# Performance work log

Hardware: AMD Instinct MI355X
Metric: run time of the kernel (lower is better)

Reference implementation:

```python
import jax, jax.numpy as jnp
import numpy as np

T, N, D, H = 128, 512, 1024, 1024
LN_EPS = 1e-5


def setup_inputs() -> dict:
    key = jax.random.key(0)
    ks = jax.random.split(key, 6)
    x = jax.random.normal(ks[0], (T * N, D), jnp.float32)
    hxs = jax.random.normal(ks[1], (N, 1, H), jnp.float32)
    # binary done-masks (float, mostly 1.0 = keep hidden state, 0.0 = episode reset)
    masks = (jax.random.uniform(ks[2], (T * N, 1)) < 0.95).astype(jnp.float32)
    s = 1.0 / np.sqrt(H)
    # PyTorch GRU packed gates, order (r, z, n): weight_ih_l0 [3H, D], weight_hh_l0 [3H, H]
    W_ih = jax.random.normal(ks[3], (3 * H, D), jnp.float32) * s
    W_hh = jax.random.normal(ks[4], (3 * H, H), jnp.float32) * s
    b_ih = jnp.zeros((3 * H,), jnp.float32)  # module inits biases to 0
    b_hh = jnp.zeros((3 * H,), jnp.float32)
    gamma = jnp.ones((H,), jnp.float32)
    beta = jnp.zeros((H,), jnp.float32)
    return dict(x=x, hxs=hxs, masks=masks, W_ih=W_ih, W_hh=W_hh,
                b_ih=b_ih, b_hh=b_hh, gamma=gamma, beta=beta)


def reference(x, hxs, masks, W_ih, W_hh, b_ih, b_hh, gamma, beta):
    TN = x.shape[0]
    Nn = hxs.shape[0]
    Tt = TN // Nn
    Hd = hxs.shape[-1]
    xs = x.reshape(Tt, Nn, -1)          # [T, N, D]
    m = masks.reshape(Tt, Nn)           # [T, N]
    # Chunk starts per source: t=0 plus every t>=1 where (masks[t] == 1).any().
    # At a chunk start the hidden state is multiplied by masks[t] (broadcast over layers);
    # a scan with a per-step conditional mask-multiply is exactly equivalent to the
    # torch loop over chunks.
    reset = jnp.concatenate([jnp.ones((1,), bool), jnp.any(m[1:] == 1.0, axis=-1)])
    # Batch the input projection across all T*N tokens (one big GEMM): [T, N, 3H]
    xp = jnp.einsum('tnd,gd->tng', xs, W_ih) + b_ih
    h0 = hxs[:, 0, :]                   # recurrent_N == 1 -> [N, H]

    def step(h, inp):
        xp_t, m_t, r_t = inp
        h = jnp.where(r_t, h * m_t[:, None], h)
        hp = h @ W_hh.T + b_hh          # [N, 3H]
        xr, xz, xn = jnp.split(xp_t, 3, axis=-1)
        hr, hz, hn = jnp.split(hp, 3, axis=-1)
        r = jax.nn.sigmoid(xr + hr)
        z = jax.nn.sigmoid(xz + hz)
        n = jnp.tanh(xn + r * hn)
        h_new = (1.0 - z) * n + z * h
        return h_new, h_new

    h_last, outs = jax.lax.scan(step, h0, (xp, m, reset))
    y = outs.reshape(Tt * Nn, Hd)
    # LayerNorm over last dim
    mu = y.mean(-1, keepdims=True)
    var = y.var(-1, keepdims=True)
    y = (y - mu) * jax.lax.rsqrt(var + LN_EPS) * gamma + beta
    return y, h_last[:, None, :]
```

## Files before the change

kernel.cpp:

```cpp
#include <hip/hip_runtime.h>

#define T_STEPS 128
#define N_B     512
#define D_IN    1024
#define H_DIM   1024
#define G_DIM   3072
#define M_ALL   (T_STEPS * N_B)
#define BAR_STRIDE 64

typedef short          s8v  __attribute__((ext_vector_type(8)));
typedef float          f4v  __attribute__((ext_vector_type(4)));
typedef unsigned short u4v  __attribute__((ext_vector_type(4)));

__device__ __forceinline__ unsigned short f2bf(float f) {
  union { float f; unsigned u; } v; v.f = f;
  unsigned r = v.u + 0x7FFFu + ((v.u >> 16) & 1u);
  return (unsigned short)(r >> 16);
}
__device__ __forceinline__ float bf2f(unsigned short h) {
  union { unsigned u; float f; } v; v.u = ((unsigned)h) << 16;
  return v.f;
}
__device__ __forceinline__ void async16(const void* g, void* l) {
  __builtin_amdgcn_global_load_lds(
      (const __attribute__((address_space(1))) unsigned*)g,
      (__attribute__((address_space(3))) unsigned*)l, 16, 0, 0);
}
__device__ __forceinline__ void async16_sc0(const void* g, void* l) {
  __builtin_amdgcn_global_load_lds(
      (const __attribute__((address_space(1))) unsigned*)g,
      (__attribute__((address_space(3))) unsigned*)l, 16, 0, 1);
}
__device__ __forceinline__ float sigmoidf_(float x) { return 1.f / (1.f + __expf(-x)); }
__device__ __forceinline__ float tanhf_(float x)    { return 1.f - 2.f / (1.f + __expf(2.f * x)); }

__global__ void cvt_bf16(const float* __restrict__ in, unsigned short* __restrict__ out, long n4) {
  long i = (long)blockIdx.x * blockDim.x + threadIdx.x;
  long stride = (long)gridDim.x * blockDim.x;
  for (; i < n4; i += stride) {
    f4v v = *(const f4v*)(in + i * 4);
    u4v o;
    #pragma unroll
    for (int e = 0; e < 4; ++e) o[e] = f2bf(v[e]);
    *(u4v*)(out + i * 4) = o;
  }
}

__global__ void reset_kernel(const float* __restrict__ masks, int* __restrict__ reset) {
  const int t = blockIdx.x;
  __shared__ int flag;
  if (threadIdx.x == 0) flag = (t == 0) ? 1 : 0;
  __syncthreads();
  if (t > 0 && masks[(size_t)t * N_B + threadIdx.x] == 1.0f) flag = 1;
  __syncthreads();
  if (threadIdx.x == 0) reset[t] = flag;
}

__global__ __launch_bounds__(256) void gemm_xp(const unsigned short* __restrict__ A,
                                               const unsigned short* __restrict__ B,
                                               const float* __restrict__ bias,
                                               unsigned short* __restrict__ C) {
  const int m0 = blockIdx.y * 128, g0 = blockIdx.x * 128;
  const int tid = threadIdx.x, wv = tid >> 6, l = tid & 63;
  const int l15 = l & 15, l4 = l >> 4;
  const int wr = wv >> 1, wc = wv & 1;
  __shared__ unsigned short As[128 * 64], Bs[128 * 64];

  f4v zero4 = {0.f, 0.f, 0.f, 0.f};
  f4v acc[4][4];
  #pragma unroll
  for (int i = 0; i < 4; ++i)
    #pragma unroll
    for (int j = 0; j < 4; ++j) acc[i][j] = zero4;

  const int srow = l >> 3;
  const int selem = ((l & 7) ^ srow) * 8;
  const int swz_rd = (l15 & 7) << 4;

  for (int kt = 0; kt < 1024; kt += 64) {
    #pragma unroll
    for (int cc = 0; cc < 4; ++cc) {
      int s = wv * 4 + cc;
      int row = s * 8 + srow;
      async16(A + (size_t)(m0 + row) * 1024 + kt + selem, &As[s * 512]);
      async16(B + (size_t)(g0 + row) * 1024 + kt + selem, &Bs[s * 512]);
    }
    __syncthreads();
    #pragma unroll
    for (int ks = 0; ks < 2; ++ks) {
      s8v a[4], b[4];
      #pragma unroll
      for (int i = 0; i < 4; ++i) {
        int ra = wr * 64 + i * 16 + l15, rb = wc * 64 + i * 16 + l15;
        int cb = (ks * 64 + l4 * 16) ^ swz_rd;
        a[i] = *(const s8v*)((const char*)As + ra * 128 + cb);
        b[i] = *(const s8v*)((const char*)Bs + rb * 128 + cb);
      }
      #pragma unroll
      for (int i = 0; i < 4; ++i)
        #pragma unroll
        for (int j = 0; j < 4; ++j)
          acc[i][j] = __builtin_amdgcn_mfma_f32_16x16x32_bf16(a[i], b[j], acc[i][j], 0, 0, 0);
    }
    __syncthreads();
  }
  #pragma unroll
  for (int j = 0; j < 4; ++j) {
    int gcol = g0 + wc * 64 + j * 16 + l15;
    float bv = bias[gcol];
    #pragma unroll
    for (int i = 0; i < 4; ++i) {
      int mrow = m0 + wr * 64 + i * 16 + l4 * 4;
      u4v o;
      #pragma unroll
      for (int r = 0; r < 4; ++r) o[r] = f2bf(acc[i][j][r] + bv);
      *(u4v*)(C + (size_t)gcol * M_ALL + mrow) = o;
    }
  }
}

__global__ __launch_bounds__(256) void rnn_chunk6(
    const unsigned short* __restrict__ Whh,
    const unsigned short* __restrict__ xpT,
    const float* __restrict__ masks,
    const int* __restrict__ reset,
    const float* __restrict__ bhh,
    const float* __restrict__ hxs,
    unsigned short* hbuf,
    float* __restrict__ y,
    float* __restrict__ hlast,
    unsigned* bar) {
  const int bid = blockIdx.x;
  const int g = bid & 7, c = bid >> 3;
  const int n0 = g * 64, j0 = c * 32;
  const int tid = threadIdx.x, w = tid >> 6, l = tid & 63;
  const int l15 = l & 15, l4 = l >> 4;
  const int wn = w & 1, wj = w >> 1;
  const size_t NH = (size_t)N_B * H_DIM;

  __shared__ unsigned short Hs[3][64 * 128];
  __shared__ unsigned short Ws[3][96 * 128];
  __shared__ unsigned short xpl[3][32][64];

  const int lrow4 = l >> 4;
  const int lcb = (l & 15) * 16;
  const int swz_rd = (l15 & 7) << 4;

  const int jj = j0 + wj * 16 + l15;
  const float br = bhh[jj];
  const float bz = bhh[H_DIM + jj];
  const float bn = bhh[2 * H_DIM + jj];

  float hreg[2][4];
  #pragma unroll
  for (int i = 0; i < 2; ++i)
    #pragma unroll
    for (int r = 0; r < 4; ++r)
      hreg[i][r] = hxs[(size_t)(n0 + wn * 32 + i * 16 + l4 * 4 + r) * H_DIM + jj];

  f4v zero4 = {0.f, 0.f, 0.f, 0.f};
  s8v zer8 = {0, 0, 0, 0, 0, 0, 0, 0};

  for (int t = 0; t < T_STEPS; ++t) {
    const unsigned short* hread = hbuf + (size_t)(t & 1) * NH;
    unsigned short* hwrite = hbuf + (size_t)((t & 1) ^ 1) * NH;
    const int rst = reset[t];

    bool zo[2];
    #pragma unroll
    for (int i = 0; i < 2; ++i) {
      float mv = masks[(size_t)t * N_B + n0 + wn * 32 + i * 16 + l15];
      zo[i] = rst && (mv == 0.0f);
    }
    float mreg[2][4];
    #pragma unroll
    for (int i = 0; i < 2; ++i)
      #pragma unroll
      for (int r = 0; r < 4; ++r)
        mreg[i][r] = masks[(size_t)t * N_B + n0 + wn * 32 + i * 16 + l4 * 4 + r];

    f4v acc[2][3];
    #pragma unroll
    for (int i = 0; i < 2; ++i)
      #pragma unroll
      for (int g3 = 0; g3 < 3; ++g3) acc[i][g3] = zero4;

    auto stage = [&](int buf, int kt) {
      #pragma unroll
      for (int q = 0; q < 4; ++q) {
        int rb = w * 16 + q * 4;
        int row = rb + lrow4;
        int cb = lcb ^ ((row & 7) << 4);
        async16_sc0(hread + (size_t)(n0 + row) * H_DIM + kt * 128 + (cb >> 1),
                    &Hs[buf][rb * 128]);
      }
      #pragma unroll
      for (int q = 0; q < 6; ++q) {
        int rb = w * 24 + q * 4;
        int row = rb + lrow4;
        int gate = row >> 5, jjl = row & 31;
        int cb = lcb ^ ((row & 7) << 4);
        async16(Whh + ((size_t)gate * H_DIM + j0 + jjl) * H_DIM + kt * 128 + (cb >> 1),
                &Ws[buf][rb * 128]);
      }
    };

    stage(0, 0); stage(1, 1); stage(2, 2);

    {
      const int jl = w * 8 + (l >> 3);
      const int nelem = ((l & 7) ^ (l >> 3)) * 8;
      #pragma unroll
      for (int g3 = 0; g3 < 3; ++g3)
        async16(xpT + (size_t)(g3 * H_DIM + j0 + jl) * M_ALL + (size_t)t * N_B + n0 + nelem,
                &xpl[g3][w * 8][0]);
    }

#define KT_BODY(KT, VM, DO_STAGE)                                              \
    {                                                                          \
      asm volatile("s_waitcnt vmcnt(" #VM ")" ::: "memory");                   \
      __builtin_amdgcn_s_barrier();                                            \
      __builtin_amdgcn_sched_barrier(0);                                       \
      if (DO_STAGE) stage((KT + 2) % 3, KT + 2);                               \
      const char* hb = (const char*)&Hs[KT % 3][0];                            \
      const char* wb = (const char*)&Ws[KT % 3][0];                            \
      _Pragma("unroll")                                                        \
      for (int ks = 0; ks < 4; ++ks) {                                         \
        const int kbb = (ks * 64 + l4 * 16) ^ swz_rd;                          \
        s8v a[2], b[3];                                                        \
        _Pragma("unroll")                                                      \
        for (int i = 0; i < 2; ++i) {                                          \
          a[i] = *(const s8v*)(hb + (wn * 32 + i * 16 + l15) * 256 + kbb);     \
          if (zo[i]) a[i] = zer8;                                              \
        }                                                                      \
        _Pragma("unroll")                                                      \
        for (int g3 = 0; g3 < 3; ++g3)                                         \
          b[g3] = *(const s8v*)(wb + (g3 * 32 + wj * 16 + l15) * 256 + kbb);   \
        _Pragma("unroll")                                                      \
        for (int i = 0; i < 2; ++i)                                            \
          _Pragma("unroll")                                                    \
          for (int g3 = 0; g3 < 3; ++g3)                                       \
            acc[i][g3] = __builtin_amdgcn_mfma_f32_16x16x32_bf16(a[i], b[g3],  \
                                                                acc[i][g3], 0, 0, 0); \
      }                                                                        \
    }

    KT_BODY(0, 23, false)
    KT_BODY(1, 13, true)
    KT_BODY(2, 13, true)
    KT_BODY(3, 10, true)
    KT_BODY(4, 10, true)
    KT_BODY(5, 10, true)
    KT_BODY(6, 10, false)
    KT_BODY(7, 0,  false)
#undef KT_BODY

    #pragma unroll
    for (int i = 0; i < 2; ++i) {
      #pragma unroll
      for (int r = 0; r < 4; ++r) {
        const int n = n0 + wn * 32 + i * 16 + l4 * 4 + r;
        const int nl = wn * 32 + i * 16 + l4 * 4 + r;
        const int jl = wj * 16 + l15;
        float hprev = hreg[i][r];
        if (rst && mreg[i][r] == 0.0f) hprev = 0.0f;
        const float hr = acc[i][0][r] + br;
        const float hz = acc[i][1][r] + bz;
        const float hn = acc[i][2][r] + bn;
        const char* xb = (const char*)&xpl[0][0][0];
        const int nb = (nl * 2) ^ ((jl & 7) << 4);
        const float xr = bf2f(*(const unsigned short*)(xb + 0 * 4096 + jl * 128 + nb));
        const float xz = bf2f(*(const unsigned short*)(xb + 1 * 4096 + jl * 128 + nb));
        const float xn = bf2f(*(const unsigned short*)(xb + 2 * 4096 + jl * 128 + nb));
        const float rg = sigmoidf_(xr + hr);
        const float zg = sigmoidf_(xz + hz);
        const float ng = tanhf_(xn + rg * hn);
        const float hnew = (1.f - zg) * ng + zg * hprev;
        hreg[i][r] = hnew;
        const size_t gidx = (size_t)n * H_DIM + jj;
        y[(size_t)t * NH + gidx] = hnew;
        hwrite[gidx] = f2bf(hnew);
        if (t == T_STEPS - 1) hlast[gidx] = hnew;
      }
    }

    __syncthreads();
    if (tid == 0) {
      __hip_atomic_fetch_add(&bar[g * BAR_STRIDE], 1u, __ATOMIC_RELAXED, __HIP_MEMORY_SCOPE_AGENT);
      const unsigned tgt = 32u * (unsigned)(t + 1);
      while (__hip_atomic_load(&bar[g * BAR_STRIDE], __ATOMIC_RELAXED, __HIP_MEMORY_SCOPE_AGENT) < tgt)
        __builtin_amdgcn_s_sleep(1);
    }
    __syncthreads();
  }
}

__global__ __launch_bounds__(256) void ln_kernel(float* __restrict__ y,
                                                 const float* __restrict__ gamma,
                                                 const float* __restrict__ beta) {
  const size_t row = blockIdx.x;
  float* p = y + row * (size_t)H_DIM;
  const int tid = threadIdx.x;
  f4v v = *(const f4v*)(p + tid * 4);
  float s = v[0] + v[1] + v[2] + v[3];
  float q = v[0] * v[0] + v[1] * v[1] + v[2] * v[2] + v[3] * v[3];
  #pragma unroll
  for (int off = 32; off > 0; off >>= 1) {
    s += __shfl_down(s, off);
    q += __shfl_down(q, off);
  }
  __shared__ float sb[8];
  const int wid = tid >> 6, lid = tid & 63;
  if (lid == 0) { sb[wid] = s; sb[4 + wid] = q; }
  __syncthreads();
  float S = sb[0] + sb[1] + sb[2] + sb[3];
  float Q = sb[4] + sb[5] + sb[6] + sb[7];
  float mean = S * (1.f / H_DIM);
  float var = Q * (1.f / H_DIM) - mean * mean;
  float inv = rsqrtf(var + 1e-5f);
  f4v g4 = *(const f4v*)(gamma + tid * 4);
  f4v b4 = *(const f4v*)(beta + tid * 4);
  f4v o;
  #pragma unroll
  for (int e = 0; e < 4; ++e) o[e] = (v[e] - mean) * inv * g4[e] + b4[e];
  *(f4v*)(p + tid * 4) = o;
}

extern "C" void kernel_launch(void* const* d_in, const int* in_sizes, int n_in,
                              void* d_out, int out_size, void* d_ws, size_t ws_size,
                              hipStream_t stream) {
  const float* x     = (const float*)d_in[0];
  const float* hxs   = (const float*)d_in[1];
  const float* masks = (const float*)d_in[2];
  const float* W_ih  = (const float*)d_in[3];
  const float* W_hh  = (const float*)d_in[4];
  const float* b_ih  = (const float*)d_in[5];
  const float* b_hh  = (const float*)d_in[6];
  const float* gamma = (const float*)d_in[7];
  const float* beta  = (const float*)d_in[8];
  float* y = (float*)d_out;
  float* hlast = y + (size_t)T_STEPS * N_B * H_DIM;

  char* ws = (char*)d_ws;
  unsigned short* Wih_bf = (unsigned short*)ws;  ws += (size_t)G_DIM * D_IN * 2;
  unsigned short* Whh_bf = (unsigned short*)ws;  ws += (size_t)G_DIM * H_DIM * 2;
  unsigned short* xc_bf  = (unsigned short*)ws;  ws += (size_t)M_ALL * D_IN * 2;
  unsigned short* xpT_bf = (unsigned short*)ws;  ws += (size_t)G_DIM * M_ALL * 2;
  unsigned short* hbuf   = (unsigned short*)ws;  ws += (size_t)2 * N_B * H_DIM * 2;
  unsigned* bars         = (unsigned*)ws;        ws += 8 * BAR_STRIDE * sizeof(unsigned);
  int* reset             = (int*)ws;             ws += 512;

  hipMemsetAsync(bars, 0, 8 * BAR_STRIDE * sizeof(unsigned), stream);
  cvt_bf16<<<1024, 256, 0, stream>>>(W_ih, Wih_bf, (long)G_DIM * D_IN / 4);
  cvt_bf16<<<1024, 256, 0, stream>>>(W_hh, Whh_bf, (long)G_DIM * H_DIM / 4);
  cvt_bf16<<<512, 256, 0, stream>>>(hxs, hbuf, (long)N_B * H_DIM / 4);
  reset_kernel<<<128, 512, 0, stream>>>(masks, reset);
  cvt_bf16<<<4096, 256, 0, stream>>>(x, xc_bf, (long)M_ALL * D_IN / 4);

  dim3 gg(G_DIM / 128, M_ALL / 128);
  gemm_xp<<<gg, 256, 0, stream>>>(xc_bf, Wih_bf, b_ih, xpT_bf);

  rnn_chunk6<<<256, 256, 0, stream>>>(Whh_bf, xpT_bf, masks, reset, b_hh,
                                      hxs, hbuf, y, hlast, bars);

  ln_kernel<<<T_STEPS * N_B, 256, 0, stream>>>(y, gamma, beta);
}
```

Before: 2.606 ms.

## Split recurrent kernel into per-chunk launches with coherent hidden-state loads/stores

The single persistent recurrent launch over all 128 steps becomes 8 launches of 16 steps each. Each launch reloads the fp32 hidden state from the previous step's output and uses its own barrier counters. Block-to-tile mapping changes so the 32 blocks that share a batch tile are contiguous in block index. Hidden-state loads and stores now use system-coherent cache bits (sc0 sc1) in place of sc0-only loads, which may bypass more cache levels. Extra launches add overhead but bound the persistent-grid spin time.

```diff
diff --git a/kernel.cpp b/kernel.cpp
--- a/kernel.cpp
+++ b/kernel.cpp
@@ -6,6 +6,8 @@
 #define H_DIM   1024
 #define G_DIM   3072
 #define M_ALL   (T_STEPS * N_B)
+#define CHUNK   16
+#define NCHUNK  8
 #define BAR_STRIDE 64
 
 typedef short          s8v  __attribute__((ext_vector_type(8)));
@@ -26,10 +28,14 @@
       (const __attribute__((address_space(1))) unsigned*)g,
       (__attribute__((address_space(3))) unsigned*)l, 16, 0, 0);
 }
-__device__ __forceinline__ void async16_sc0(const void* g, void* l) {
+__device__ __forceinline__ void async16_coh(const void* g, void* l) {
   __builtin_amdgcn_global_load_lds(
       (const __attribute__((address_space(1))) unsigned*)g,
-      (__attribute__((address_space(3))) unsigned*)l, 16, 0, 1);
+      (__attribute__((address_space(3))) unsigned*)l, 16, 0, 17);
+}
+__device__ __forceinline__ void store_bf16_coh(unsigned short* p, unsigned short v) {
+  unsigned v32 = v;
+  asm volatile("global_store_short %0, %1, off sc0 sc1" :: "v"(p), "v"(v32) : "memory");
 }
 __device__ __forceinline__ float sigmoidf_(float x) { return 1.f / (1.f + __expf(-x)); }
 __device__ __forceinline__ float tanhf_(float x)    { return 1.f - 2.f / (1.f + __expf(2.f * x)); }
@@ -119,7 +125,7 @@
   }
 }
 
-__global__ __launch_bounds__(256) void rnn_chunk6(
+__global__ __launch_bounds__(256) void rnn_chunk7(
     const unsigned short* __restrict__ Whh,
     const unsigned short* __restrict__ xpT,
     const float* __restrict__ masks,
@@ -129,10 +135,11 @@
     unsigned short* hbuf,
     float* __restrict__ y,
     float* __restrict__ hlast,
-    unsigned* bar) {
+    unsigned* bar,
+    int t0) {
   const int bid = blockIdx.x;
-  const int g = bid & 7, c = bid >> 3;
-  const int n0 = g * 64, j0 = c * 32;
+  const int jt = bid & 31, nt = bid >> 5;
+  const int j0 = jt * 32, n0 = nt * 64;
   const int tid = threadIdx.x, w = tid >> 6, l = tid & 63;
   const int l15 = l & 15, l4 = l >> 4;
   const int wn = w & 1, wj = w >> 1;
@@ -152,16 +159,20 @@
   const float bn = bhh[2 * H_DIM + jj];
 
   float hreg[2][4];
-  #pragma unroll
-  for (int i = 0; i < 2; ++i)
-    #pragma unroll
-    for (int r = 0; r < 4; ++r)
-      hreg[i][r] = hxs[(size_t)(n0 + wn * 32 + i * 16 + l4 * 4 + r) * H_DIM + jj];
+  {
+    const float* hsrc = (t0 == 0) ? hxs : (y + (size_t)(t0 - 1) * NH);
+    #pragma unroll
+    for (int i = 0; i < 2; ++i)
+      #pragma unroll
+      for (int r = 0; r < 4; ++r)
+        hreg[i][r] = hsrc[(size_t)(n0 + wn * 32 + i * 16 + l4 * 4 + r) * H_DIM + jj];
+  }
 
   f4v zero4 = {0.f, 0.f, 0.f, 0.f};
   s8v zer8 = {0, 0, 0, 0, 0, 0, 0, 0};
 
-  for (int t = 0; t < T_STEPS; ++t) {
+  for (int ls = 0; ls < CHUNK; ++ls) {
+    const int t = t0 + ls;
     const unsigned short* hread = hbuf + (size_t)(t & 1) * NH;
     unsigned short* hwrite = hbuf + (size_t)((t & 1) ^ 1) * NH;
     const int rst = reset[t];
@@ -191,7 +202,7 @@
         int rb = w * 16 + q * 4;
         int row = rb + lrow4;
         int cb = lcb ^ ((row & 7) << 4);
-        async16_sc0(hread + (size_t)(n0 + row) * H_DIM + kt * 128 + (cb >> 1),
+        async16_coh(hread + (size_t)(n0 + row) * H_DIM + kt * 128 + (cb >> 1),
                     &Hs[buf][rb * 128]);
       }
       #pragma unroll
@@ -279,16 +290,16 @@
         hreg[i][r] = hnew;
         const size_t gidx = (size_t)n * H_DIM + jj;
         y[(size_t)t * NH + gidx] = hnew;
-        hwrite[gidx] = f2bf(hnew);
+        store_bf16_coh(hwrite + gidx, f2bf(hnew));
         if (t == T_STEPS - 1) hlast[gidx] = hnew;
       }
     }
 
     __syncthreads();
     if (tid == 0) {
-      __hip_atomic_fetch_add(&bar[g * BAR_STRIDE], 1u, __ATOMIC_RELAXED, __HIP_MEMORY_SCOPE_AGENT);
-      const unsigned tgt = 32u * (unsigned)(t + 1);
-      while (__hip_atomic_load(&bar[g * BAR_STRIDE], __ATOMIC_RELAXED, __HIP_MEMORY_SCOPE_AGENT) < tgt)
+      __hip_atomic_fetch_add(&bar[nt * BAR_STRIDE], 1u, __ATOMIC_RELAXED, __HIP_MEMORY_SCOPE_AGENT);
+      const unsigned tgt = 32u * (unsigned)(ls + 1);
+      while (__hip_atomic_load(&bar[nt * BAR_STRIDE], __ATOMIC_RELAXED, __HIP_MEMORY_SCOPE_AGENT) < tgt)
         __builtin_amdgcn_s_sleep(1);
     }
     __syncthreads();
@@ -347,10 +358,10 @@
   unsigned short* xc_bf  = (unsigned short*)ws;  ws += (size_t)M_ALL * D_IN * 2;
   unsigned short* xpT_bf = (unsigned short*)ws;  ws += (size_t)G_DIM * M_ALL * 2;
   unsigned short* hbuf   = (unsigned short*)ws;  ws += (size_t)2 * N_B * H_DIM * 2;
-  unsigned* bars         = (unsigned*)ws;        ws += 8 * BAR_STRIDE * sizeof(unsigned);
+  unsigned* bars         = (unsigned*)ws;        ws += NCHUNK * 8 * BAR_STRIDE * sizeof(unsigned);
   int* reset             = (int*)ws;             ws += 512;
 
-  hipMemsetAsync(bars, 0, 8 * BAR_STRIDE * sizeof(unsigned), stream);
+  hipMemsetAsync(bars, 0, NCHUNK * 8 * BAR_STRIDE * sizeof(unsigned), stream);
   cvt_bf16<<<1024, 256, 0, stream>>>(W_ih, Wih_bf, (long)G_DIM * D_IN / 4);
   cvt_bf16<<<1024, 256, 0, stream>>>(W_hh, Whh_bf, (long)G_DIM * H_DIM / 4);
   cvt_bf16<<<512, 256, 0, stream>>>(hxs, hbuf, (long)N_B * H_DIM / 4);
@@ -360,8 +371,11 @@
   dim3 gg(G_DIM / 128, M_ALL / 128);
   gemm_xp<<<gg, 256, 0, stream>>>(xc_bf, Wih_bf, b_ih, xpT_bf);
 
-  rnn_chunk6<<<256, 256, 0, stream>>>(Whh_bf, xpT_bf, masks, reset, b_hh,
-                                      hxs, hbuf, y, hlast, bars);
+  for (int ck = 0; ck < NCHUNK; ++ck) {
+    rnn_chunk7<<<256, 256, 0, stream>>>(Whh_bf, xpT_bf, masks, reset, b_hh, hxs, hbuf,
+                                        y, hlast, bars + (size_t)ck * 8 * BAR_STRIDE,
+                                        ck * CHUNK);
+  }
 
   ln_kernel<<<T_STEPS * N_B, 256, 0, stream>>>(y, gamma, beta);
 }
```

Result: faster. 2.287 ms (-12.2%).
